# Performance work log

Measured on AMD Instinct MI355X. Metric: run time of the kernel, lower is better.

## Reference

```python
import jax, jax.numpy as jnp
import numpy as np

WS = 4            # window_size
C = 192           # dim
NH = 6            # num_heads
HD = C // NH      # head_dim
HID = 384         # mlp hidden = int(dim * mlp_ratio)
EPS = 1e-5


def _rel_pos_index(ws):
    coords = np.stack(np.meshgrid(np.arange(ws), np.arange(ws), np.arange(ws), indexing='ij'))  # [3,ws,ws,ws]
    cf = coords.reshape(3, -1)                                # [3, N]
    rel = cf[:, :, None] - cf[:, None, :]                     # [3, N, N]
    rel = rel.transpose(1, 2, 0)                              # [N, N, 3]
    rel += ws - 1
    rel[:, :, 0] *= (2 * ws - 1) * (2 * ws - 1)
    rel[:, :, 1] *= 2 * ws - 1
    return jnp.asarray(rel.sum(-1), dtype=jnp.int32)          # [N, N]

REL_IDX = _rel_pos_index(WS)


def setup_inputs() -> dict:
    key = jax.random.key(0)
    ks = jax.random.split(key, 20)
    s = 0.02
    B, Dd, Hh, Ww = 2, 48, 48, 48
    L = Dd * Hh * Ww
    tbl = (2 * WS - 1) ** 3
    return {
        'x': jax.random.normal(ks[0], (B, L, C), jnp.float32),
        'D': Dd, 'H': Hh, 'W': Ww,
        'ln1_g': jnp.ones((C,), jnp.float32), 'ln1_b': jnp.zeros((C,), jnp.float32),
        'ln2_g': jnp.ones((C,), jnp.float32), 'ln2_b': jnp.zeros((C,), jnp.float32),
        'qkv_w': jax.random.normal(ks[1], (C, 3 * C), jnp.float32) * s,
        'qkv_b': jnp.zeros((3 * C,), jnp.float32),
        'rpb_table': jax.random.normal(ks[2], (tbl, NH), jnp.float32) * s,
        'proj_w': jax.random.normal(ks[3], (C, C), jnp.float32) * s,
        'proj_b': jnp.zeros((C,), jnp.float32),
        'fc1_w': jax.random.normal(ks[4], (C, HID), jnp.float32) * s,
        'fc1_b': jnp.zeros((HID,), jnp.float32),
        'dw_w': jax.random.normal(ks[5], (HID, 1, 3, 3, 3), jnp.float32) * s,
        'dw_b': jnp.zeros((HID,), jnp.float32),
        'bn_g': jnp.ones((HID,), jnp.float32), 'bn_b': jnp.zeros((HID,), jnp.float32),
        'bn_mean': jnp.zeros((HID,), jnp.float32), 'bn_var': jnp.ones((HID,), jnp.float32),
        'fc2_w': jax.random.normal(ks[6], (HID, C), jnp.float32) * s,
        'fc2_b': jnp.zeros((C,), jnp.float32),
    }


def _ln(x, g, b):
    m = jnp.mean(x, -1, keepdims=True)
    v = jnp.mean((x - m) ** 2, -1, keepdims=True)
    return (x - m) * jax.lax.rsqrt(v + EPS) * g + b


def _window_attn(xw, qkv_w, qkv_b, rpb_table, proj_w, proj_b):
    # xw: [nW, N, C]
    nW, N, _ = xw.shape
    qkv = (xw @ qkv_w + qkv_b).reshape(nW, N, 3, NH, HD)
    q, k, v = qkv[:, :, 0], qkv[:, :, 1], qkv[:, :, 2]   # [nW, N, NH, HD]
    scale = HD ** -0.5
    attn = jnp.einsum('wnhd,wmhd->whnm', q * scale, k)    # [nW, NH, N, N]
    bias = rpb_table[REL_IDX]                              # [N, N, NH]
    attn = attn + jnp.transpose(bias, (2, 0, 1))[None]
    attn = jax.nn.softmax(attn, axis=-1)
    out = jnp.einsum('whnm,wmhd->wnhd', attn, v).reshape(nW, N, C)
    return out @ proj_w + proj_b


def reference(x, D, H, W, ln1_g, ln1_b, ln2_g, ln2_b, qkv_w, qkv_b, rpb_table,
              proj_w, proj_b, fc1_w, fc1_b, dw_w, dw_b, bn_g, bn_b, bn_mean,
              bn_var, fc2_w, fc2_b):
    B, L, _ = x.shape
    shortcut = x
    # --- windowed attention ---
    xs = _ln(x, ln1_g, ln1_b).reshape(B, D, H, W, C)
    # D,H,W divisible by WS -> no padding
    xs = xs.reshape(B, D // WS, WS, H // WS, WS, W // WS, WS, C)
    xw = jnp.transpose(xs, (0, 1, 3, 5, 2, 4, 6, 7)).reshape(-1, WS ** 3, C)
    aw = _window_attn(xw, qkv_w, qkv_b, rpb_table, proj_w, proj_b)
    aw = aw.reshape(B, D // WS, H // WS, W // WS, WS, WS, WS, C)
    xr = jnp.transpose(aw, (0, 1, 4, 2, 5, 3, 6, 7)).reshape(B, L, C)
    x = shortcut + xr
    # --- efficient MLP: fc1 -> dwconv3d -> BN(eval) -> GELU -> fc2 ---
    y = _ln(x, ln2_g, ln2_b)
    h = y @ fc1_w + fc1_b                                  # [B, L, HID]
    hs = jnp.transpose(h, (0, 2, 1)).reshape(B, HID, D, H, W)
    hs = jax.lax.conv_general_dilated(
        hs, dw_w, window_strides=(1, 1, 1), padding='SAME',
        feature_group_count=HID,
        dimension_numbers=('NCDHW', 'OIDHW', 'NCDHW')) + dw_b[None, :, None, None, None]
    hs = (hs - bn_mean[None, :, None, None, None]) * jax.lax.rsqrt(
        bn_var[None, :, None, None, None] + EPS) * bn_g[None, :, None, None, None] + bn_b[None, :, None, None, None]
    h = jnp.transpose(hs.reshape(B, HID, L), (0, 2, 1))
    h = jax.nn.gelu(h, approximate=False)
    return x + (h @ fc2_w + fc2_b)
```

## Files before the change

### kernel.cpp

```cpp
#include <hip/hip_runtime.h>

typedef __bf16 bf16;
typedef __bf16 bf16x8 __attribute__((ext_vector_type(8)));
typedef float f32x4 __attribute__((ext_vector_type(4)));

#define L_TOT 110592
#define TOKS  221184
#define NWIN  3456

static __device__ __forceinline__ f32x4 mfma16(bf16x8 a, bf16x8 b, f32x4 c) {
    return __builtin_amdgcn_mfma_f32_16x16x32_bf16(a, b, c, 0, 0, 0);
}
static __device__ __forceinline__ bf16x8 ld8(const bf16* p) { return *(const bf16x8*)p; }

__global__ void wt_transpose(const float* __restrict__ src, bf16* __restrict__ dst, int K, int N) {
    int i = blockIdx.x * 256 + threadIdx.x;
    if (i >= K * N) return;
    int n = i / K, k = i - n * K;
    dst[i] = (bf16)src[k * N + n];
}

__global__ void bias6_build(const float* __restrict__ rpb, float* __restrict__ bias6) {
    int i = blockIdx.x * 256 + threadIdx.x;
    if (i >= 6 * 64 * 64) return;
    int h = i >> 12, n = (i >> 6) & 63, m = i & 63;
    int r0 = (n >> 4) - (m >> 4) + 3;
    int r1 = ((n >> 2) & 3) - ((m >> 2) & 3) + 3;
    int r2 = (n & 3) - (m & 3) + 3;
    bias6[i] = rpb[(r0 * 49 + r1 * 7 + r2) * 6 + h];
}

__global__ void ln1_window(const float* __restrict__ x, const float* __restrict__ g,
                           const float* __restrict__ bt, bf16* __restrict__ xw) {
    int wave = threadIdx.x >> 6, lane = threadIdx.x & 63;
    int t = blockIdx.x * 4 + wave;
    const float* row = x + (long)t * 192;
    float v0 = row[lane], v1 = row[lane + 64], v2 = row[lane + 128];
    float s = v0 + v1 + v2;
    #pragma unroll
    for (int m = 1; m < 64; m <<= 1) s += __shfl_xor(s, m);
    float mu = s * (1.0f / 192.0f);
    float d0 = v0 - mu, d1 = v1 - mu, d2 = v2 - mu;
    float q = d0 * d0 + d1 * d1 + d2 * d2;
    #pragma unroll
    for (int m = 1; m < 64; m <<= 1) q += __shfl_xor(q, m);
    float r = rsqrtf(q * (1.0f / 192.0f) + 1e-5f);
    int b = t / L_TOT, l = t - b * L_TOT;
    int dz = l / 2304, rem = l - dz * 2304;
    int hy = rem / 48, wx = rem - hy * 48;
    int w = ((b * 12 + (dz >> 2)) * 12 + (hy >> 2)) * 12 + (wx >> 2);
    int n = (dz & 3) * 16 + (hy & 3) * 4 + (wx & 3);
    bf16* o = xw + ((long)(w * 64 + n)) * 192;
    o[lane]       = (bf16)(d0 * r * g[lane]       + bt[lane]);
    o[lane + 64]  = (bf16)(d1 * r * g[lane + 64]  + bt[lane + 64]);
    o[lane + 128] = (bf16)(d2 * r * g[lane + 128] + bt[lane + 128]);
}

__global__ void ln2_kernel(const bf16* __restrict__ in, const float* __restrict__ g,
                           const float* __restrict__ bt, bf16* __restrict__ y) {
    int wave = threadIdx.x >> 6, lane = threadIdx.x & 63;
    long t = blockIdx.x * 4 + wave;
    const bf16* row = in + t * 192;
    float v0 = (float)row[lane], v1 = (float)row[lane + 64], v2 = (float)row[lane + 128];
    float s = v0 + v1 + v2;
    #pragma unroll
    for (int m = 1; m < 64; m <<= 1) s += __shfl_xor(s, m);
    float mu = s * (1.0f / 192.0f);
    float d0 = v0 - mu, d1 = v1 - mu, d2 = v2 - mu;
    float q = d0 * d0 + d1 * d1 + d2 * d2;
    #pragma unroll
    for (int m = 1; m < 64; m <<= 1) q += __shfl_xor(q, m);
    float r = rsqrtf(q * (1.0f / 192.0f) + 1e-5f);
    bf16* o = y + t * 192;
    o[lane]       = (bf16)(d0 * r * g[lane]       + bt[lane]);
    o[lane + 64]  = (bf16)(d1 * r * g[lane + 64]  + bt[lane + 64]);
    o[lane + 128] = (bf16)(d2 * r * g[lane + 128] + bt[lane + 128]);
}

__global__ __launch_bounds__(256) void gemm_qkv(
    const bf16* __restrict__ xw, const bf16* __restrict__ wt,
    const float* __restrict__ bqkv,
    bf16* __restrict__ qb, bf16* __restrict__ kb_, bf16* __restrict__ vtb) {
    int m0 = blockIdx.x * 128;
    int wid = threadIdx.x >> 6, lane = threadIdx.x & 63;
    int wr = wid >> 1, wc = wid & 1;
    int lo = lane & 15, hi = lane >> 4;
    f32x4 zf = {0.f, 0.f, 0.f, 0.f};

    const bf16* Ab = xw + (long)(m0 + wr * 64 + lo) * 192 + hi * 8;
    bf16x8 a[4][6];
    #pragma unroll
    for (int ti = 0; ti < 4; ++ti)
        #pragma unroll
        for (int ks = 0; ks < 6; ++ks)
            a[ti][ks] = ld8(Ab + ti * 16 * 192 + ks * 32);

    #pragma unroll
    for (int nc = 0; nc < 9; ++nc) {
        int sect = nc / 3;
        int cb0 = (nc - sect * 3) * 64;
        f32x4 acc[4][2];
        #pragma unroll
        for (int i = 0; i < 4; ++i) { acc[i][0] = zf; acc[i][1] = zf; }
        const bf16* Bb = wt + (long)(nc * 64 + wc * 32 + lo) * 192 + hi * 8;
        #pragma unroll
        for (int ks = 0; ks < 6; ++ks) {
            bf16x8 b0 = ld8(Bb + ks * 32);
            bf16x8 b1 = ld8(Bb + 16 * 192 + ks * 32);
            #pragma unroll
            for (int ti = 0; ti < 4; ++ti) {
                acc[ti][0] = mfma16(a[ti][ks], b0, acc[ti][0]);
                acc[ti][1] = mfma16(a[ti][ks], b1, acc[ti][1]);
            }
        }
        #pragma unroll
        for (int ti = 0; ti < 4; ++ti)
            #pragma unroll
            for (int j = 0; j < 4; ++j) {
                int trow = m0 + wr * 64 + ti * 16 + hi * 4 + j;
                int w = trow >> 6, n = trow & 63;
                #pragma unroll
                for (int tj = 0; tj < 2; ++tj) {
                    int cw = cb0 + wc * 32 + tj * 16 + lo;
                    int h = cw >> 5, d = cw & 31;
                    float val = acc[ti][tj][j] + bqkv[sect * 192 + cw];
                    long wh = (long)(w * 6 + h);
                    if (sect == 0)       qb[(wh * 64 + n) * 32 + d] = (bf16)(val * 0.17677669529663687f);
                    else if (sect == 1)  kb_[(wh * 64 + n) * 32 + d] = (bf16)val;
                    else                 vtb[(wh * 32 + d) * 64 + n] = (bf16)val;
                }
            }
    }
}

__global__ __launch_bounds__(384) void attn_light(
    const bf16* __restrict__ qb, const bf16* __restrict__ kb_,
    const bf16* __restrict__ vtb, const float* __restrict__ bias6,
    bf16* __restrict__ aw) {
    __shared__ char p_smem[6 * 8192];
    int w = blockIdx.x;
    int h = threadIdx.x >> 6;
    int lane = threadIdx.x & 63;
    int lo = lane & 15, hi = lane >> 4;
    char* ph = p_smem + h * 8192;
    long wh = (long)(w * 6 + h);
    f32x4 zf = {0.f, 0.f, 0.f, 0.f};

    bf16x8 qa[4], kb[4];
    #pragma unroll
    for (int ti = 0; ti < 4; ++ti) qa[ti] = ld8(qb  + (wh * 64 + ti * 16 + lo) * 32 + hi * 8);
    #pragma unroll
    for (int tj = 0; tj < 4; ++tj) kb[tj] = ld8(kb_ + (wh * 64 + tj * 16 + lo) * 32 + hi * 8);
    f32x4 s[4][4];
    #pragma unroll
    for (int ti = 0; ti < 4; ++ti)
        #pragma unroll
        for (int tj = 0; tj < 4; ++tj)
            s[ti][tj] = mfma16(qa[ti], kb[tj], zf);

    const float* bh = bias6 + h * 4096;
    #pragma unroll
    for (int ti = 0; ti < 4; ++ti)
        #pragma unroll
        for (int j = 0; j < 4; ++j) {
            int rr = ti * 16 + hi * 4 + j;
            float ev[4];
            #pragma unroll
            for (int tj = 0; tj < 4; ++tj) s[ti][tj][j] += bh[rr * 64 + tj * 16 + lo];
            float mx = fmaxf(fmaxf(s[ti][0][j], s[ti][1][j]), fmaxf(s[ti][2][j], s[ti][3][j]));
            #pragma unroll
            for (int m = 1; m < 16; m <<= 1) mx = fmaxf(mx, __shfl_xor(mx, m));
            float sum = 0.f;
            #pragma unroll
            for (int tj = 0; tj < 4; ++tj) { ev[tj] = __expf(s[ti][tj][j] - mx); sum += ev[tj]; }
            #pragma unroll
            for (int m = 1; m < 16; m <<= 1) sum += __shfl_xor(sum, m);
            float inv = 1.0f / sum;
            #pragma unroll
            for (int tj = 0; tj < 4; ++tj) {
                int byte = ((rr * 64 + tj * 16 + lo) * 2) ^ ((rr & 7) << 4);
                *(bf16*)(ph + byte) = (bf16)(ev[tj] * inv);
            }
        }

    f32x4 o[4][2];
    #pragma unroll
    for (int i = 0; i < 4; ++i) { o[i][0] = zf; o[i][1] = zf; }
    #pragma unroll
    for (int ks2 = 0; ks2 < 2; ++ks2) {
        bf16x8 pa[4], vb[2];
        #pragma unroll
        for (int ti = 0; ti < 4; ++ti) {
            int row = ti * 16 + lo;
            pa[ti] = *(const bf16x8*)(ph + ((row * 128 + ks2 * 64 + hi * 16) ^ ((row & 7) << 4)));
        }
        #pragma unroll
        for (int td = 0; td < 2; ++td)
            vb[td] = ld8(vtb + (wh * 32 + td * 16 + lo) * 64 + ks2 * 32 + hi * 8);
        #pragma unroll
        for (int ti = 0; ti < 4; ++ti)
            #pragma unroll
            for (int td = 0; td < 2; ++td)
                o[ti][td] = mfma16(pa[ti], vb[td], o[ti][td]);
    }
    bf16* orow = aw + (long)w * 64 * 192 + h * 32;
    #pragma unroll
    for (int ti = 0; ti < 4; ++ti)
        #pragma unroll
        for (int td = 0; td < 2; ++td)
            #pragma unroll
            for (int j = 0; j < 4; ++j)
                orow[(ti * 16 + hi * 4 + j) * 192 + td * 16 + lo] = (bf16)o[ti][td][j];
}

__global__ __launch_bounds__(256) void gemm_proj(
    const bf16* __restrict__ aw, const bf16* __restrict__ wt,
    const float* __restrict__ bias, const float* __restrict__ x,
    bf16* __restrict__ out1) {
    int m0 = blockIdx.x * 128;
    int wid = threadIdx.x >> 6, lane = threadIdx.x & 63;
    int wr = wid >> 1, wc = wid & 1;
    int lo = lane & 15, hi = lane >> 4;
    f32x4 zf = {0.f, 0.f, 0.f, 0.f};

    const bf16* Ab = aw + (long)(m0 + wr * 64 + lo) * 192 + hi * 8;
    bf16x8 a[4][6];
    #pragma unroll
    for (int ti = 0; ti < 4; ++ti)
        #pragma unroll
        for (int ks = 0; ks < 6; ++ks)
            a[ti][ks] = ld8(Ab + ti * 16 * 192 + ks * 32);

    #pragma unroll
    for (int nc = 0; nc < 3; ++nc) {
        f32x4 acc[4][2];
        #pragma unroll
        for (int i = 0; i < 4; ++i) { acc[i][0] = zf; acc[i][1] = zf; }
        const bf16* Bb = wt + (long)(nc * 64 + wc * 32 + lo) * 192 + hi * 8;
        #pragma unroll
        for (int ks = 0; ks < 6; ++ks) {
            bf16x8 b0 = ld8(Bb + ks * 32);
            bf16x8 b1 = ld8(Bb + 16 * 192 + ks * 32);
            #pragma unroll
            for (int ti = 0; ti < 4; ++ti) {
                acc[ti][0] = mfma16(a[ti][ks], b0, acc[ti][0]);
                acc[ti][1] = mfma16(a[ti][ks], b1, acc[ti][1]);
            }
        }
        #pragma unroll
        for (int ti = 0; ti < 4; ++ti)
            #pragma unroll
            for (int j = 0; j < 4; ++j) {
                int trow = m0 + wr * 64 + ti * 16 + hi * 4 + j;
                int wv = trow >> 6, n = trow & 63;
                int bb = wv / 1728; int rem = wv - bb * 1728;
                int dq = rem / 144; int rem2 = rem - dq * 144;
                int hq = rem2 / 12; int wq = rem2 - hq * 12;
                int l = (dq * 4 + (n >> 4)) * 2304 + (hq * 4 + ((n >> 2) & 3)) * 48 + (wq * 4 + (n & 3));
                long base = ((long)bb * L_TOT + l) * 192;
                #pragma unroll
                for (int tj = 0; tj < 2; ++tj) {
                    int col = nc * 64 + wc * 32 + tj * 16 + lo;
                    out1[base + col] = (bf16)(x[base + col] + acc[ti][tj][j] + bias[col]);
                }
            }
    }
}

__global__ __launch_bounds__(256) void gemm_fc1(
    const bf16* __restrict__ y, const bf16* __restrict__ wt,
    const float* __restrict__ bias, bf16* __restrict__ h_t) {
    __shared__ bf16 tl[64][136];
    int m0 = blockIdx.x * 128;
    int wid = threadIdx.x >> 6, lane = threadIdx.x & 63;
    int wr = wid >> 1, wc = wid & 1;
    int lo = lane & 15, hi = lane >> 4;
    f32x4 zf = {0.f, 0.f, 0.f, 0.f};
    int bb = m0 / L_TOT; int l0 = m0 - bb * L_TOT;
    int col = threadIdx.x >> 2, seg = threadIdx.x & 3;

    const bf16* Ab = y + (long)(m0 + wr * 64 + lo) * 192 + hi * 8;
    bf16x8 a[4][6];
    #pragma unroll
    for (int ti = 0; ti < 4; ++ti)
        #pragma unroll
        for (int ks = 0; ks < 6; ++ks)
            a[ti][ks] = ld8(Ab + ti * 16 * 192 + ks * 32);

    #pragma unroll
    for (int nc = 0; nc < 6; ++nc) {
        f32x4 acc[4][2];
        #pragma unroll
        for (int i = 0; i < 4; ++i) { acc[i][0] = zf; acc[i][1] = zf; }
        const bf16* Bb = wt + (long)(nc * 64 + wc * 32 + lo) * 192 + hi * 8;
        #pragma unroll
        for (int ks = 0; ks < 6; ++ks) {
            bf16x8 b0 = ld8(Bb + ks * 32);
            bf16x8 b1 = ld8(Bb + 16 * 192 + ks * 32);
            #pragma unroll
            for (int ti = 0; ti < 4; ++ti) {
                acc[ti][0] = mfma16(a[ti][ks], b0, acc[ti][0]);
                acc[ti][1] = mfma16(a[ti][ks], b1, acc[ti][1]);
            }
        }
        if (nc) __syncthreads();
        #pragma unroll
        for (int ti = 0; ti < 4; ++ti)
            #pragma unroll
            for (int tj = 0; tj < 2; ++tj)
                #pragma unroll
                for (int j = 0; j < 4; ++j) {
                    int rl = wr * 64 + ti * 16 + hi * 4 + j;
                    int cl = wc * 32 + tj * 16 + lo;
                    tl[cl][rl] = (bf16)(acc[ti][tj][j] + bias[nc * 64 + cl]);
                }
        __syncthreads();
        bf16* dst = h_t + ((long)bb * 384 + nc * 64 + col) * L_TOT + l0 + seg * 32;
        #pragma unroll
        for (int i8 = 0; i8 < 4; ++i8)
            *(bf16x8*)(dst + i8 * 8) = *(const bf16x8*)(&tl[col][seg * 32 + i8 * 8]);
    }
}

__global__ __launch_bounds__(320) void dwconv_bn_gelu(
    const bf16* __restrict__ h_t, const float* __restrict__ wconv,
    const float* __restrict__ cb, const float* __restrict__ bng,
    const float* __restrict__ bnb, const float* __restrict__ bnm,
    const float* __restrict__ bnv, bf16* __restrict__ g_t) {
    __shared__ __align__(16) bf16 tile[289 * 56];
    int blk = blockIdx.x;
    int bb = blk / 4608; int rem = blk - bb * 4608;
    int ch = rem / 12; int zb = rem - ch * 12; int z0 = zb * 4;
    const bf16* src = h_t + ((long)bb * 384 + ch) * L_TOT;

    uint4 zv = make_uint4(0u, 0u, 0u, 0u);
    for (int i = threadIdx.x; i < 295; i += 320) {
        int e = (i < 7) ? i * 8 : ((i - 7 + 1) * 56 + 48);
        *(uint4*)(tile + e) = zv;
    }
    for (int c = threadIdx.x; c < 1728; c += 320) {
        int zi = c / 288; int rc = c - zi * 288;
        int r = rc / 6; int cx8 = rc - r * 6;
        int gz = z0 - 1 + zi;
        uint4 val = zv;
        if (gz >= 0 && gz < 48) val = *(const uint4*)(src + (long)gz * 2304 + r * 48 + cx8 * 8);
        *(uint4*)(tile + (1 + zi * 48 + r) * 56 + cx8 * 8) = val;
    }
    float wgt[27];
    #pragma unroll
    for (int i = 0; i < 27; ++i) wgt[i] = wconv[ch * 27 + i];
    float scale = bng[ch] * rsqrtf(bnv[ch] + 1e-5f);
    float shift = bnb[ch] - bnm[ch] * scale;
    float cbias = cb[ch];
    __syncthreads();

    if (threadIdx.x < 288) {
        int y = threadIdx.x / 6, cx = threadIdx.x - y * 6, x0 = cx * 8;
        __builtin_assume(y < 48);
        bool up_ok = (y > 0), dn_ok = (y < 47);
        bf16* dstc = g_t + ((long)bb * 384 + ch) * L_TOT + (long)z0 * 2304 + y * 48 + x0;
        float acc[4][8];
        #pragma unroll
        for (int p = 0; p < 4; ++p)
            #pragma unroll
            for (int k = 0; k < 8; ++k) acc[p][k] = 0.f;

        #pragma unroll
        for (int zi = 0; zi < 6; ++zi) {
            const bf16* plane = tile + (1 + zi * 48) * 56;
            #pragma unroll
            for (int dy = 0; dy < 3; ++dy) {
                bool ok = (dy == 1) || (dy == 0 ? up_ok : dn_ok);
                if (ok) {
                    const bf16* rp = plane + (y + dy - 1) * 56 + x0;
                    bf16x8 mv = ld8(rp);
                    float s[10];
                    s[0] = (float)rp[-1];
                    #pragma unroll
                    for (int i = 0; i < 8; ++i) s[i + 1] = (float)mv[i];
                    s[9] = (float)rp[8];
                    #pragma unroll
                    for (int dz = 0; dz < 3; ++dz) {
                        int p = zi - dz;
                        if (p >= 0 && p <= 3) {
                            float w0 = wgt[dz * 9 + dy * 3 + 0];
                            float w1 = wgt[dz * 9 + dy * 3 + 1];
                            float w2 = wgt[dz * 9 + dy * 3 + 2];
                            #pragma unroll
                            for (int k = 0; k < 8; ++k)
                                acc[p][k] = fmaf(w0, s[k], fmaf(w1, s[k + 1], fmaf(w2, s[k + 2], acc[p][k])));
                        }
                    }
                }
            }
            if (zi >= 2) {
                int p = zi - 2;
                bf16x8 ov;
                #pragma unroll
                for (int k = 0; k < 8; ++k) {
                    float v = acc[p][k] + cbias;
                    v = fmaf(v, scale, shift);
                    float v2 = v * v;
                    float u2 = v * fmaf(v2, 0.0713548162726f, 1.5957691216057308f);
                    float e  = __expf(u2);
                    float q  = __builtin_amdgcn_rcpf(e + 1.0f);
                    ov[k] = (bf16)(v - v * q);
                }
                *(bf16x8*)(dstc + p * 2304) = ov;
            }
        }
    }
}

__global__ __launch_bounds__(256) void gemm_fc2(
    const bf16* __restrict__ g_t, const bf16* __restrict__ wt,
    const float* __restrict__ bias, const bf16* __restrict__ out1,
    float* __restrict__ out) {
    __shared__ bf16 As[2][4096];
    int m0 = blockIdx.x * 64;
    int wc = threadIdx.x >> 6, lane = threadIdx.x & 63;
    int lo = lane & 15, hi = lane >> 4;
    int bb = m0 / L_TOT, l0 = m0 - bb * L_TOT;
    f32x4 zf = {0.f, 0.f, 0.f, 0.f};
    f32x4 acc[3][4];
    #pragma unroll
    for (int tj = 0; tj < 3; ++tj)
        #pragma unroll
        for (int ti = 0; ti < 4; ++ti) acc[tj][ti] = zf;

    int sch = threadIdx.x >> 3;
    int seg = threadIdx.x & 7;
    const bf16* srcb = g_t + ((long)bb * 384 + sch) * L_TOT + l0 + seg * 8;

    bf16x8 r[2];
    #pragma unroll
    for (int p = 0; p < 2; ++p) r[p] = ld8(srcb + (long)(p * 32) * L_TOT);
    #pragma unroll
    for (int p = 0; p < 2; ++p)
        #pragma unroll
        for (int i = 0; i < 8; ++i)
            As[0][(seg * 8 + i) * 64 + ((p * 32 + sch) ^ (((seg ^ i) & 7) << 3))] = r[p][i];

    #pragma unroll
    for (int t = 0; t < 6; ++t) {
        __syncthreads();
        if (t < 5) {
            #pragma unroll
            for (int p = 0; p < 2; ++p)
                r[p] = ld8(srcb + (long)((t + 1) * 64 + p * 32) * L_TOT);
        }
        const bf16* Ac = As[t & 1];
        #pragma unroll
        for (int ksin = 0; ksin < 2; ++ksin) {
            bf16x8 a[4];
            #pragma unroll
            for (int ti = 0; ti < 4; ++ti) {
                int rr = ti * 16 + lo;
                int S = ((rr >> 3) ^ rr) & 7;
                a[ti] = *(const bf16x8*)&Ac[rr * 64 + ((ksin * 32 + hi * 8) ^ (S << 3))];
            }
            #pragma unroll
            for (int tj = 0; tj < 3; ++tj) {
                bf16x8 b0 = ld8(wt + (long)(wc * 48 + tj * 16 + lo) * 384 + t * 64 + ksin * 32 + hi * 8);
                #pragma unroll
                for (int ti = 0; ti < 4; ++ti)
                    acc[tj][ti] = mfma16(a[ti], b0, acc[tj][ti]);
            }
        }
        if (t < 5) {
            bf16* An = As[(t + 1) & 1];
            #pragma unroll
            for (int p = 0; p < 2; ++p)
                #pragma unroll
                for (int i = 0; i < 8; ++i)
                    An[(seg * 8 + i) * 64 + ((p * 32 + sch) ^ (((seg ^ i) & 7) << 3))] = r[p][i];
        }
    }
    #pragma unroll
    for (int tj = 0; tj < 3; ++tj)
        #pragma unroll
        for (int ti = 0; ti < 4; ++ti)
            #pragma unroll
            for (int j = 0; j < 4; ++j) {
                long trow = m0 + ti * 16 + hi * 4 + j;
                long base = trow * 192;
                int col = wc * 48 + tj * 16 + lo;
                out[base + col] = (float)out1[base + col] + acc[tj][ti][j] + bias[col];
            }
}

extern "C" void kernel_launch(void* const* d_in, const int* in_sizes, int n_in,
                              void* d_out, int out_size, void* d_ws, size_t ws_size,
                              hipStream_t stream) {
    (void)in_sizes; (void)n_in; (void)out_size; (void)ws_size;
    const float* x     = (const float*)d_in[0];
    const float* ln1g  = (const float*)d_in[4];
    const float* ln1b  = (const float*)d_in[5];
    const float* ln2g  = (const float*)d_in[6];
    const float* ln2b  = (const float*)d_in[7];
    const float* qkvw  = (const float*)d_in[8];
    const float* qkvb  = (const float*)d_in[9];
    const float* rpb   = (const float*)d_in[10];
    const float* projw = (const float*)d_in[11];
    const float* projb = (const float*)d_in[12];
    const float* fc1w  = (const float*)d_in[13];
    const float* fc1b  = (const float*)d_in[14];
    const float* dww   = (const float*)d_in[15];
    const float* dwb   = (const float*)d_in[16];
    const float* bng   = (const float*)d_in[17];
    const float* bnb   = (const float*)d_in[18];
    const float* bnm   = (const float*)d_in[19];
    const float* bnv   = (const float*)d_in[20];
    const float* fc2w  = (const float*)d_in[21];
    const float* fc2b  = (const float*)d_in[22];
    float* out = (float*)d_out;

    char* ws = (char*)d_ws;
    size_t o = 0;
    bf16*  out1 = (bf16*)(ws + o);
    bf16*  vt_buf = (bf16*)(ws + o + 84934656); o += 169869312;
    bf16*  h_t  = (bf16*)(ws + o); o += 169869312;
    bf16*  region1 = (bf16*)(ws + o); o += 169869312;
    bf16*  xw  = region1;
    bf16*  aw  = region1 + 42467328;
    bf16*  yb  = region1;
    bf16*  g_t = region1;
    bf16*  qkvwt  = (bf16*)(ws + o); o += 221184;
    bf16*  projwt = (bf16*)(ws + o); o += 73728;
    bf16*  fc1wt  = (bf16*)(ws + o); o += 147456;
    bf16*  fc2wt  = (bf16*)(ws + o); o += 147456;
    float* bias6  = (float*)(ws + o); o += 98304;

    bf16* q_buf  = h_t;
    bf16* k_buf  = h_t + 42467328;

    wt_transpose<<<(110592 + 255) / 256, 256, 0, stream>>>(qkvw, qkvwt, 192, 576);
    wt_transpose<<<(36864 + 255) / 256, 256, 0, stream>>>(projw, projwt, 192, 192);
    wt_transpose<<<(73728 + 255) / 256, 256, 0, stream>>>(fc1w, fc1wt, 192, 384);
    wt_transpose<<<(73728 + 255) / 256, 256, 0, stream>>>(fc2w, fc2wt, 384, 192);
    bias6_build<<<96, 256, 0, stream>>>(rpb, bias6);

    ln1_window<<<55296, 256, 0, stream>>>(x, ln1g, ln1b, xw);
    gemm_qkv<<<1728, 256, 0, stream>>>(xw, qkvwt, qkvb, q_buf, k_buf, vt_buf);
    attn_light<<<NWIN, 384, 0, stream>>>(q_buf, k_buf, vt_buf, bias6, aw);
    gemm_proj<<<1728, 256, 0, stream>>>(aw, projwt, projb, x, out1);
    ln2_kernel<<<55296, 256, 0, stream>>>(out1, ln2g, ln2b, yb);
    gemm_fc1<<<1728, 256, 0, stream>>>(yb, fc1wt, fc1b, h_t);
    dwconv_bn_gelu<<<9216, 320, 0, stream>>>(h_t, dww, dwb, bng, bnb, bnm, bnv, g_t);
    gemm_fc2<<<3456, 256, 0, stream>>>(g_t, fc2wt, fc2b, out1, out);
}
```

Baseline: 861.8 us.

## Store activations and weights in MFMA fragment-blocked layout across kernels

```diff
diff --git a/kernel.cpp b/kernel.cpp
--- a/kernel.cpp
+++ b/kernel.cpp
@@ -13,10 +13,13 @@
 }
 static __device__ __forceinline__ bf16x8 ld8(const bf16* p) { return *(const bf16x8*)p; }
 
-__global__ void wt_transpose(const float* __restrict__ src, bf16* __restrict__ dst, int K, int N) {
+__global__ void wt_frag(const float* __restrict__ src, bf16* __restrict__ dst, int K, int N) {
     int i = blockIdx.x * 256 + threadIdx.x;
     if (i >= K * N) return;
-    int n = i / K, k = i - n * K;
+    int kw = i & 31, col = (i >> 5) & 63, rest = i >> 11;
+    int nks = K >> 5;
+    int ks = rest % nks, chunk = rest / nks;
+    int n = chunk * 64 + col, k = ks * 32 + kw;
     dst[i] = (bf16)src[k * N + n];
 }
 
@@ -50,10 +53,10 @@
     int hy = rem / 48, wx = rem - hy * 48;
     int w = ((b * 12 + (dz >> 2)) * 12 + (hy >> 2)) * 12 + (wx >> 2);
     int n = (dz & 3) * 16 + (hy & 3) * 4 + (wx & 3);
-    bf16* o = xw + ((long)(w * 64 + n)) * 192;
-    o[lane]       = (bf16)(d0 * r * g[lane]       + bt[lane]);
-    o[lane + 64]  = (bf16)(d1 * r * g[lane + 64]  + bt[lane + 64]);
-    o[lane + 128] = (bf16)(d2 * r * g[lane + 128] + bt[lane + 128]);
+    bf16* o = xw + (long)w * 12288 + (lane >> 5) * 2048 + n * 32 + (lane & 31);
+    o[0]    = (bf16)(d0 * r * g[lane]       + bt[lane]);
+    o[4096] = (bf16)(d1 * r * g[lane + 64]  + bt[lane + 64]);
+    o[8192] = (bf16)(d2 * r * g[lane + 128] + bt[lane + 128]);
 }
 
 __global__ void ln2_kernel(const bf16* __restrict__ in, const float* __restrict__ g,
@@ -71,10 +74,10 @@
     #pragma unroll
     for (int m = 1; m < 64; m <<= 1) q += __shfl_xor(q, m);
     float r = rsqrtf(q * (1.0f / 192.0f) + 1e-5f);
-    bf16* o = y + t * 192;
-    o[lane]       = (bf16)(d0 * r * g[lane]       + bt[lane]);
-    o[lane + 64]  = (bf16)(d1 * r * g[lane + 64]  + bt[lane + 64]);
-    o[lane + 128] = (bf16)(d2 * r * g[lane + 128] + bt[lane + 128]);
+    bf16* o = y + (t >> 6) * 12288 + (lane >> 5) * 2048 + (t & 63) * 32 + (lane & 31);
+    o[0]    = (bf16)(d0 * r * g[lane]       + bt[lane]);
+    o[4096] = (bf16)(d1 * r * g[lane + 64]  + bt[lane + 64]);
+    o[8192] = (bf16)(d2 * r * g[lane + 128] + bt[lane + 128]);
 }
 
 __global__ __launch_bounds__(256) void gemm_qkv(
@@ -82,18 +85,19 @@
     const float* __restrict__ bqkv,
     bf16* __restrict__ qb, bf16* __restrict__ kb_, bf16* __restrict__ vtb) {
     int m0 = blockIdx.x * 128;
+    int w0 = m0 >> 6;
     int wid = threadIdx.x >> 6, lane = threadIdx.x & 63;
     int wr = wid >> 1, wc = wid & 1;
     int lo = lane & 15, hi = lane >> 4;
     f32x4 zf = {0.f, 0.f, 0.f, 0.f};
 
-    const bf16* Ab = xw + (long)(m0 + wr * 64 + lo) * 192 + hi * 8;
+    const bf16* Ab = xw + (long)(w0 + wr) * 12288 + (lo * 32 + hi * 8);
     bf16x8 a[4][6];
     #pragma unroll
     for (int ti = 0; ti < 4; ++ti)
         #pragma unroll
         for (int ks = 0; ks < 6; ++ks)
-            a[ti][ks] = ld8(Ab + ti * 16 * 192 + ks * 32);
+            a[ti][ks] = ld8(Ab + ks * 2048 + ti * 512);
 
     #pragma unroll
     for (int nc = 0; nc < 9; ++nc) {
@@ -102,11 +106,11 @@
         f32x4 acc[4][2];
         #pragma unroll
         for (int i = 0; i < 4; ++i) { acc[i][0] = zf; acc[i][1] = zf; }
-        const bf16* Bb = wt + (long)(nc * 64 + wc * 32 + lo) * 192 + hi * 8;
+        const bf16* Bb = wt + (long)nc * 12288 + (wc * 32 + lo) * 32 + hi * 8;
         #pragma unroll
         for (int ks = 0; ks < 6; ++ks) {
-            bf16x8 b0 = ld8(Bb + ks * 32);
-            bf16x8 b1 = ld8(Bb + 16 * 192 + ks * 32);
+            bf16x8 b0 = ld8(Bb + ks * 2048);
+            bf16x8 b1 = ld8(Bb + ks * 2048 + 512);
             #pragma unroll
             for (int ti = 0; ti < 4; ++ti) {
                 acc[ti][0] = mfma16(a[ti][ks], b0, acc[ti][0]);
@@ -203,14 +207,14 @@
             for (int td = 0; td < 2; ++td)
                 o[ti][td] = mfma16(pa[ti], vb[td], o[ti][td]);
     }
-    bf16* orow = aw + (long)w * 64 * 192 + h * 32;
+    bf16* orow = aw + wh * 2048;
     #pragma unroll
     for (int ti = 0; ti < 4; ++ti)
         #pragma unroll
         for (int td = 0; td < 2; ++td)
             #pragma unroll
             for (int j = 0; j < 4; ++j)
-                orow[(ti * 16 + hi * 4 + j) * 192 + td * 16 + lo] = (bf16)o[ti][td][j];
+                orow[(ti * 16 + hi * 4 + j) * 32 + td * 16 + lo] = (bf16)o[ti][td][j];
 }
 
 __global__ __launch_bounds__(256) void gemm_proj(
@@ -218,29 +222,30 @@
     const float* __restrict__ bias, const float* __restrict__ x,
     bf16* __restrict__ out1) {
     int m0 = blockIdx.x * 128;
+    int w0 = m0 >> 6;
     int wid = threadIdx.x >> 6, lane = threadIdx.x & 63;
     int wr = wid >> 1, wc = wid & 1;
     int lo = lane & 15, hi = lane >> 4;
     f32x4 zf = {0.f, 0.f, 0.f, 0.f};
 
-    const bf16* Ab = aw + (long)(m0 + wr * 64 + lo) * 192 + hi * 8;
+    const bf16* Ab = aw + (long)(w0 + wr) * 12288 + (lo * 32 + hi * 8);
     bf16x8 a[4][6];
     #pragma unroll
     for (int ti = 0; ti < 4; ++ti)
         #pragma unroll
         for (int ks = 0; ks < 6; ++ks)
-            a[ti][ks] = ld8(Ab + ti * 16 * 192 + ks * 32);
+            a[ti][ks] = ld8(Ab + ks * 2048 + ti * 512);
 
     #pragma unroll
     for (int nc = 0; nc < 3; ++nc) {
         f32x4 acc[4][2];
         #pragma unroll
         for (int i = 0; i < 4; ++i) { acc[i][0] = zf; acc[i][1] = zf; }
-        const bf16* Bb = wt + (long)(nc * 64 + wc * 32 + lo) * 192 + hi * 8;
+        const bf16* Bb = wt + (long)nc * 12288 + (wc * 32 + lo) * 32 + hi * 8;
         #pragma unroll
         for (int ks = 0; ks < 6; ++ks) {
-            bf16x8 b0 = ld8(Bb + ks * 32);
-            bf16x8 b1 = ld8(Bb + 16 * 192 + ks * 32);
+            bf16x8 b0 = ld8(Bb + ks * 2048);
+            bf16x8 b1 = ld8(Bb + ks * 2048 + 512);
             #pragma unroll
             for (int ti = 0; ti < 4; ++ti) {
                 acc[ti][0] = mfma16(a[ti][ks], b0, acc[ti][0]);
@@ -272,6 +277,7 @@
     const float* __restrict__ bias, bf16* __restrict__ h_t) {
     __shared__ bf16 tl[64][136];
     int m0 = blockIdx.x * 128;
+    int c0 = m0 >> 6;
     int wid = threadIdx.x >> 6, lane = threadIdx.x & 63;
     int wr = wid >> 1, wc = wid & 1;
     int lo = lane & 15, hi = lane >> 4;
@@ -279,24 +285,24 @@
     int bb = m0 / L_TOT; int l0 = m0 - bb * L_TOT;
     int col = threadIdx.x >> 2, seg = threadIdx.x & 3;
 
-    const bf16* Ab = y + (long)(m0 + wr * 64 + lo) * 192 + hi * 8;
+    const bf16* Ab = y + (long)(c0 + wr) * 12288 + (lo * 32 + hi * 8);
     bf16x8 a[4][6];
     #pragma unroll
     for (int ti = 0; ti < 4; ++ti)
         #pragma unroll
         for (int ks = 0; ks < 6; ++ks)
-            a[ti][ks] = ld8(Ab + ti * 16 * 192 + ks * 32);
+            a[ti][ks] = ld8(Ab + ks * 2048 + ti * 512);
 
     #pragma unroll
     for (int nc = 0; nc < 6; ++nc) {
         f32x4 acc[4][2];
         #pragma unroll
         for (int i = 0; i < 4; ++i) { acc[i][0] = zf; acc[i][1] = zf; }
-        const bf16* Bb = wt + (long)(nc * 64 + wc * 32 + lo) * 192 + hi * 8;
+        const bf16* Bb = wt + (long)nc * 12288 + (wc * 32 + lo) * 32 + hi * 8;
         #pragma unroll
         for (int ks = 0; ks < 6; ++ks) {
-            bf16x8 b0 = ld8(Bb + ks * 32);
-            bf16x8 b1 = ld8(Bb + 16 * 192 + ks * 32);
+            bf16x8 b0 = ld8(Bb + ks * 2048);
+            bf16x8 b1 = ld8(Bb + ks * 2048 + 512);
             #pragma unroll
             for (int ti = 0; ti < 4; ++ti) {
                 acc[ti][0] = mfma16(a[ti][ks], b0, acc[ti][0]);
@@ -461,7 +467,9 @@
             }
             #pragma unroll
             for (int tj = 0; tj < 3; ++tj) {
-                bf16x8 b0 = ld8(wt + (long)(wc * 48 + tj * 16 + lo) * 384 + t * 64 + ksin * 32 + hi * 8);
+                int cstart = wc * 48 + tj * 16;
+                b16_load:;
+                bf16x8 b0 = ld8(wt + ((long)((cstart >> 6) * 12 + t * 2 + ksin) * 64 + (cstart & 63) + lo) * 32 + hi * 8);
                 #pragma unroll
                 for (int ti = 0; ti < 4; ++ti)
                     acc[tj][ti] = mfma16(a[ti], b0, acc[tj][ti]);
@@ -534,10 +542,10 @@
     bf16* q_buf  = h_t;
     bf16* k_buf  = h_t + 42467328;
 
-    wt_transpose<<<(110592 + 255) / 256, 256, 0, stream>>>(qkvw, qkvwt, 192, 576);
-    wt_transpose<<<(36864 + 255) / 256, 256, 0, stream>>>(projw, projwt, 192, 192);
-    wt_transpose<<<(73728 + 255) / 256, 256, 0, stream>>>(fc1w, fc1wt, 192, 384);
-    wt_transpose<<<(73728 + 255) / 256, 256, 0, stream>>>(fc2w, fc2wt, 384, 192);
+    wt_frag<<<(110592 + 255) / 256, 256, 0, stream>>>(qkvw, qkvwt, 192, 576);
+    wt_frag<<<(36864 + 255) / 256, 256, 0, stream>>>(projw, projwt, 192, 192);
+    wt_frag<<<(73728 + 255) / 256, 256, 0, stream>>>(fc1w, fc1wt, 192, 384);
+    wt_frag<<<(73728 + 255) / 256, 256, 0, stream>>>(fc2w, fc2wt, 384, 192);
     bias6_build<<<96, 256, 0, stream>>>(rpb, bias6);
 
     ln1_window<<<55296, 256, 0, stream>>>(x, ln1g, ln1b, xw);
```

Result: faster. 756.8 us (-12.2%).
